# Performance work log

Measured on AMD Instinct MI355X. Metric: run time of the kernel, lower is better.

Reference implementation:

```python
import jax, jax.numpy as jnp
import numpy as np

D_MODEL = 2048
N_HEADS = 16
HEAD_DIM = D_MODEL // N_HEADS
SEGMENT_SIZE = 512
DILATION = 2
BATCH = 2
SEQ_LEN = 8192


def setup_inputs() -> dict:
    key = jax.random.key(0)
    k1, k2, k3 = jax.random.split(key, 3)
    x = jax.random.normal(k1, (BATCH, SEQ_LEN, D_MODEL), dtype=jnp.float32)
    Wqkv = jax.random.normal(k2, (3 * D_MODEL, D_MODEL), dtype=jnp.float32) * 0.02
    b_qkv = jnp.zeros((3 * D_MODEL,), dtype=jnp.float32)
    Wout = jax.random.normal(k3, (D_MODEL, D_MODEL), dtype=jnp.float32) * 0.02
    b_out = jnp.zeros((D_MODEL,), dtype=jnp.float32)
    return {"x": x, "Wqkv": Wqkv, "b_qkv": b_qkv, "Wout": Wout, "b_out": b_out}


def reference(x, Wqkv, b_qkv, Wout, b_out):
    B, S, D = x.shape
    H, hd = N_HEADS, HEAD_DIM
    # dilated segment gather: [B, n_seg, seg, D] strided by dilation -> [B, n_seg, L, D]
    xs = x.reshape(B, -1, SEGMENT_SIZE, D)[:, :, ::DILATION, :]
    N, L = xs.shape[1], xs.shape[2]
    # fused qkv projection (FlashMHA.Wqkv)
    qkv = jnp.einsum('bnld,ed->bnle', xs, Wqkv) + b_qkv  # [B,N,L,3D]
    q, k, v = jnp.split(qkv, 3, axis=-1)
    q = q.reshape(B, N, L, H, hd)
    k = k.reshape(B, N, L, H, hd)
    v = v.reshape(B, N, L, H, hd)
    scale = 1.0 / jnp.sqrt(jnp.asarray(hd, dtype=x.dtype))
    # per-segment attention over the dilated tokens
    scores = jnp.einsum('bnqhd,bnkhd->bnhqk', q, k) * scale  # [B,N,H,L,L]
    attn = jax.nn.softmax(scores, axis=-1)
    out = jnp.einsum('bnhqk,bnkhd->bnqhd', attn, v).reshape(B, N, L, D)
    # output projection (FlashMHA.out_proj)
    out = jnp.einsum('bnld,ed->bnle', out, Wout) + b_out
    # merge segments back: [B, N*L, D]
    return out.reshape(B, -1, D)
```

## Files before the change

### kernel.cpp

```cpp
#include <hip/hip_runtime.h>
#include <hip/hip_bf16.h>
#include <stdint.h>

#define DEVI __device__ __forceinline__

typedef __attribute__((ext_vector_type(8))) short bf16x8;
typedef __attribute__((ext_vector_type(4))) float f32x4;


DEVI unsigned short f2bf(float f) {
  unsigned int u = __float_as_uint(f);
  return (unsigned short)((u + 0x7fffu + ((u >> 16) & 1u)) >> 16);
}

DEVI void load_lds16(const void* g, void* l) {
  __builtin_amdgcn_global_load_lds(
      (const __attribute__((address_space(1))) unsigned int*)g,
      (__attribute__((address_space(3))) unsigned int*)l, 16, 0, 0);
}

DEVI bf16x8 ld8(const unsigned short* p) {
  return *reinterpret_cast<const bf16x8*>(p);
}

__global__ void k_gather(const float* __restrict__ x, unsigned short* __restrict__ xs) {
  int i = blockIdx.x * 256 + threadIdx.x;
  int r = i >> 9;
  int c = (i & 511) << 2;
  int b = r >> 12;
  int rem = r & 4095;
  int seg = rem >> 8;
  int lcl = rem & 255;
  long src_row = (long)b * 8192 + seg * 512 + lcl * 2;
  const float4 v = *reinterpret_cast<const float4*>(x + src_row * 2048 + c);
  uint2 o;
  o.x = f2bf(v.x) | ((unsigned)f2bf(v.y) << 16);
  o.y = f2bf(v.z) | ((unsigned)f2bf(v.w) << 16);
  *reinterpret_cast<uint2*>(xs + (long)r * 2048 + c) = o;
}

__global__ void k_cast(const float* __restrict__ in, unsigned short* __restrict__ out, int n4) {
  int i = blockIdx.x * 256 + threadIdx.x;
  if (i >= n4) return;
  const float4 v = *reinterpret_cast<const float4*>(in + (long)i * 4);
  uint2 o;
  o.x = f2bf(v.x) | ((unsigned)f2bf(v.y) << 16);
  o.y = f2bf(v.z) | ((unsigned)f2bf(v.w) << 16);
  *reinterpret_cast<uint2*>(out + (long)i * 4) = o;
}


DEVI void stage_piece(const unsigned short* gb, int K, int h, int op,
                      unsigned short* smem, int t, int w) {
  char* base = (char*)(smem + (h & 3) * 16384 + op * 8192);
#pragma unroll
  for (int i = 0; i < 2; ++i) {
    int s = i * 512 + t;
    int prow = s >> 3;
    int cs8 = s & 7;
    int c8 = cs8 ^ (prow & 7);
    int r = prow * 2 + (c8 >> 2);
    int k0 = (c8 & 3) << 3;
    load_lds16(gb + (long)r * K + h * 32 + k0, base + i * 8192 + w * 1024);
  }
}

#define FRAG_A(dst, mm)                                                      \
  { int r_ = wm * 128 + (mm) * 16 + lr;                                      \
    int p_ = r_ >> 1;                                                        \
    int cs_ = (((r_ & 1) << 2) | lq) ^ (p_ & 7);                             \
    dst = ld8(Ab_ + p_ * 64 + cs_ * 8); }
#define FRAG_B(dst, nn)                                                      \
  { int r_ = wn * 64 + (nn) * 16 + lr;                                       \
    int p_ = r_ >> 1;                                                        \
    int cs_ = (((r_ & 1) << 2) | lq) ^ (p_ & 7);                             \
    dst = ld8(Bb_ + p_ * 64 + cs_ * 8); }
#define MM(mm, areg)                                                         \
  acc[mm][0] = __builtin_amdgcn_mfma_f32_16x16x32_bf16(areg, bf0, acc[mm][0], 0, 0, 0); \
  acc[mm][1] = __builtin_amdgcn_mfma_f32_16x16x32_bf16(areg, bf1, acc[mm][1], 0, 0, 0); \
  acc[mm][2] = __builtin_amdgcn_mfma_f32_16x16x32_bf16(areg, bf2, acc[mm][2], 0, 0, 0); \
  acc[mm][3] = __builtin_amdgcn_mfma_f32_16x16x32_bf16(areg, bf3, acc[mm][3], 0, 0, 0);

#define HALF(HEXPR, DOSTAGE, VMLIT)                                          \
  {                                                                          \
    const int h_ = (HEXPR);                                                  \
    const unsigned short* Ab_ = smem + (h_ & 3) * 16384;                     \
    const unsigned short* Bb_ = Ab_ + 8192;                                  \
    bf16x8 af0, af1, af2, af3, bf0, bf1, bf2, bf3;                           \
    FRAG_B(bf0, 0) FRAG_B(bf1, 1) FRAG_B(bf2, 2) FRAG_B(bf3, 3)              \
    FRAG_A(af0, 0) FRAG_A(af1, 1) FRAG_A(af2, 2) FRAG_A(af3, 3)              \
    if (DOSTAGE) stage_piece(Agb, K, h_ + 2, 0, smem, t, w);                 \
    __builtin_amdgcn_s_barrier();                                            \
    asm volatile("s_waitcnt lgkmcnt(0)" ::: "memory");                       \
    __builtin_amdgcn_sched_barrier(0);                                       \
    __builtin_amdgcn_s_setprio(1);                                           \
    MM(0, af0) MM(1, af1) MM(2, af2) MM(3, af3)                              \
    __builtin_amdgcn_s_setprio(0);                                           \
    __builtin_amdgcn_s_barrier();                                            \
    FRAG_A(af0, 4) FRAG_A(af1, 5) FRAG_A(af2, 6) FRAG_A(af3, 7)              \
    if (DOSTAGE) stage_piece(Bgb, K, h_ + 2, 1, smem, t, w);                 \
    __builtin_amdgcn_s_barrier();                                            \
    asm volatile("s_waitcnt lgkmcnt(0)" ::: "memory");                       \
    __builtin_amdgcn_sched_barrier(0);                                       \
    __builtin_amdgcn_s_setprio(1);                                           \
    MM(4, af0) MM(5, af1) MM(6, af2) MM(7, af3)                              \
    __builtin_amdgcn_s_setprio(0);                                           \
    asm volatile("s_waitcnt vmcnt(" VMLIT ")" ::: "memory");                 \
    __builtin_amdgcn_s_barrier();                                            \
  }

template <bool BF16_OUT>
__global__ __launch_bounds__(512, 1)
void k_gemm(const unsigned short* __restrict__ A, const unsigned short* __restrict__ B,
            const float* __restrict__ bias, void* __restrict__ Cv, int N, int K) {
  __shared__ unsigned short smem[65536];
  const int nbx = N >> 8;
  const int cpx = gridDim.x >> 3;
  const int id = blockIdx.x;
  const int sw = (id & 7) * cpx + (id >> 3);
  const int bx = sw % nbx, by = sw / nbx;
  const int t = threadIdx.x, w = t >> 6, l = t & 63;
  const int lr = l & 15, lq = l >> 4;
  const int wm = w >> 2, wn = w & 3;
  const unsigned short* Agb = A + (long)by * 256 * K;
  const unsigned short* Bgb = B + (long)bx * 256 * K;
  const int nh = K >> 5;
  f32x4 acc[8][4] = {};

  stage_piece(Agb, K, 0, 0, smem, t, w);
  stage_piece(Bgb, K, 0, 1, smem, t, w);
  stage_piece(Agb, K, 1, 0, smem, t, w);
  stage_piece(Bgb, K, 1, 1, smem, t, w);
  asm volatile("s_waitcnt vmcnt(4)" ::: "memory");
  __builtin_amdgcn_s_barrier();

  for (int h = 0; h < nh - 2; ++h) HALF(h, true, "4")
  HALF(nh - 2, false, "0")
  HALF(nh - 1, false, "0")

  const long crow0 = (long)by * 256 + wm * 128;
  const int ccol0 = bx * 256 + wn * 64;
  float bv[4];
#pragma unroll
  for (int n = 0; n < 4; ++n) bv[n] = bias[ccol0 + n * 16 + lr];
  const int lrr = l >> 2;
  if (BF16_OUT) {
    unsigned short* Lw = smem + w * 1216;
    const int lcb = (l & 3) * 8;
#pragma unroll
    for (int m = 0; m < 8; ++m) {
#pragma unroll
      for (int n = 0; n < 4; ++n)
#pragma unroll
        for (int r = 0; r < 4; ++r)
          Lw[(lq * 4 + r) * 76 + n * 16 + lr] = f2bf(acc[m][n][r] + bv[n]);
      asm volatile("s_waitcnt lgkmcnt(0)" ::: "memory");
#pragma unroll
      for (int rd = 0; rd < 2; ++rd) {
        bf16x8 v = ld8(Lw + lrr * 76 + lcb + rd * 32);
        *reinterpret_cast<bf16x8*>((unsigned short*)Cv +
            (crow0 + m * 16 + lrr) * N + ccol0 + lcb + rd * 32) = v;
      }
    }
  } else {
    float* Lf = (float*)smem + w * 1216;
    const int lcf = (l & 3) * 4;
#pragma unroll
    for (int m = 0; m < 8; ++m) {
#pragma unroll
      for (int n = 0; n < 4; ++n)
#pragma unroll
        for (int r = 0; r < 4; ++r)
          Lf[(lq * 4 + r) * 76 + n * 16 + lr] = acc[m][n][r] + bv[n];
      asm volatile("s_waitcnt lgkmcnt(0)" ::: "memory");
#pragma unroll
      for (int rd = 0; rd < 4; ++rd) {
        float4 v = *reinterpret_cast<const float4*>(Lf + lrr * 76 + lcf + rd * 16);
        *reinterpret_cast<float4*>((float*)Cv +
            (crow0 + m * 16 + lrr) * N + ccol0 + lcf + rd * 16) = v;
      }
    }
  }
}

__global__ __launch_bounds__(512)
void k_attn(const unsigned short* __restrict__ qkv, unsigned short* __restrict__ aout) {
  __shared__ unsigned short smem[65536];
  unsigned short* Kl = smem;
  unsigned short* Vt = smem + 32768;
  const int p = blockIdx.x;
  const int h = p & 15;
  const long rb = (long)(p >> 4) * 256;
  const int t = threadIdx.x, w = t >> 6, l = t & 63;
  const int lr = l & 15, lq = l >> 4;

  const unsigned short* kb = qkv + rb * 6144 + 2048 + h * 128;
#pragma unroll
  for (int i = 0; i < 8; ++i) {
    int s = i * 512 + t;
    int row = s >> 4;
    int ch = (s & 15) ^ (row & 7);
    load_lds16(kb + (long)row * 6144 + ch * 8, (char*)Kl + i * 8192 + w * 1024);
  }
  const unsigned short* vb = qkv + rb * 6144 + 4096 + h * 128;
#pragma unroll
  for (int j0 = 0; j0 < 8; ++j0) {
    int k = j0 * 32 + (t >> 4);
    int d0 = (t & 15) * 8;
    bf16x8 v = ld8(vb + (long)k * 6144 + d0);
#pragma unroll
    for (int j = 0; j < 8; ++j) {
      int d = d0 + j;
      int ch = (k >> 3) ^ ((d ^ (d >> 3)) & 7);
      Vt[d * 256 + ch * 8 + (k & 7)] = (unsigned short)(short)v[j];
    }
  }
  const unsigned short* qb = qkv + (rb + w * 32) * 6144 + h * 128;
  bf16x8 qa[2][4];
#pragma unroll
  for (int m = 0; m < 2; ++m)
#pragma unroll
    for (int kt = 0; kt < 4; ++kt)
      qa[m][kt] = ld8(qb + (long)(m * 16 + lr) * 6144 + kt * 32 + lq * 8);

  __syncthreads();

  f32x4 sacc[2][16] = {};
#pragma unroll
  for (int n = 0; n < 16; ++n) {
    int row = n * 16 + lr;
#pragma unroll
    for (int kt = 0; kt < 4; ++kt) {
      int ch = (kt * 4 + lq) ^ (row & 7);
      bf16x8 kf = ld8(Kl + row * 128 + ch * 8);
      sacc[0][n] = __builtin_amdgcn_mfma_f32_16x16x32_bf16(qa[0][kt], kf, sacc[0][n], 0, 0, 0);
      sacc[1][n] = __builtin_amdgcn_mfma_f32_16x16x32_bf16(qa[1][kt], kf, sacc[1][n], 0, 0, 0);
    }
  }
  const float scale = 0.08838834764831845f;
  float mx[2][4], sm[2][4];
#pragma unroll
  for (int m = 0; m < 2; ++m)
#pragma unroll
    for (int r = 0; r < 4; ++r) {
      float v = sacc[m][0][r];
#pragma unroll
      for (int n = 1; n < 16; ++n) v = fmaxf(v, sacc[m][n][r]);
      mx[m][r] = v;
      sm[m][r] = 0.f;
    }
#pragma unroll
  for (int mk = 1; mk < 16; mk <<= 1)
#pragma unroll
    for (int m = 0; m < 2; ++m)
#pragma unroll
      for (int r = 0; r < 4; ++r)
        mx[m][r] = fmaxf(mx[m][r], __shfl_xor(mx[m][r], mk));
#pragma unroll
  for (int m = 0; m < 2; ++m)
#pragma unroll
    for (int n = 0; n < 16; ++n)
#pragma unroll
      for (int r = 0; r < 4; ++r) {
        float e = __expf((sacc[m][n][r] - mx[m][r]) * scale);
        sacc[m][n][r] = e;
        sm[m][r] += e;
      }
#pragma unroll
  for (int mk = 1; mk < 16; mk <<= 1)
#pragma unroll
    for (int m = 0; m < 2; ++m)
#pragma unroll
      for (int r = 0; r < 4; ++r)
        sm[m][r] += __shfl_xor(sm[m][r], mk);
  float ri[2][4];
#pragma unroll
  for (int m = 0; m < 2; ++m)
#pragma unroll
    for (int r = 0; r < 4; ++r) ri[m][r] = 1.0f / sm[m][r];

  unsigned int pb[2][16][2];
#pragma unroll
  for (int m = 0; m < 2; ++m)
#pragma unroll
    for (int n = 0; n < 16; ++n) {
      pb[m][n][0] = f2bf(sacc[m][n][0] * ri[m][0]) | ((unsigned)f2bf(sacc[m][n][1] * ri[m][1]) << 16);
      pb[m][n][1] = f2bf(sacc[m][n][2] * ri[m][2]) | ((unsigned)f2bf(sacc[m][n][3] * ri[m][3]) << 16);
    }

  __syncthreads();
  unsigned short* Pl = Kl + w * 4096;
  f32x4 oacc[2][8] = {};
#pragma unroll
  for (int half = 0; half < 2; ++half) {
#pragma unroll
    for (int m = 0; m < 2; ++m)
#pragma unroll
      for (int n = 0; n < 8; ++n) {
        int col = n * 16 + lr;
        int row0 = m * 16 + lq * 4;
#pragma unroll
        for (int pr = 0; pr < 2; ++pr) {
          unsigned int u = pb[m][half * 8 + n][pr];
          int ra = row0 + pr * 2, rbw = ra + 1;
          int ca = (col >> 3) ^ (ra & 7);
          int cb = (col >> 3) ^ (rbw & 7);
          Pl[ra * 128 + ca * 8 + (col & 7)] = (unsigned short)(u & 0xffffu);
          Pl[rbw * 128 + cb * 8 + (col & 7)] = (unsigned short)(u >> 16);
        }
      }
#pragma unroll
    for (int kt = 0; kt < 4; ++kt) {
      bf16x8 pa[2];
#pragma unroll
      for (int m = 0; m < 2; ++m) {
        int row = m * 16 + lr;
        int ch = (kt * 4 + lq) ^ (row & 7);
        pa[m] = ld8(Pl + row * 128 + ch * 8);
      }
#pragma unroll
      for (int dt = 0; dt < 8; ++dt) {
        int d = dt * 16 + lr;
        int kg = half * 128 + kt * 32 + lq * 8;
        int ch = (kg >> 3) ^ ((d ^ (d >> 3)) & 7);
        bf16x8 vf = ld8(Vt + d * 256 + ch * 8);
        oacc[0][dt] = __builtin_amdgcn_mfma_f32_16x16x32_bf16(pa[0], vf, oacc[0][dt], 0, 0, 0);
        oacc[1][dt] = __builtin_amdgcn_mfma_f32_16x16x32_bf16(pa[1], vf, oacc[1][dt], 0, 0, 0);
      }
    }
  }
  unsigned short* ob = aout + (rb + w * 32) * 2048 + h * 128;
#pragma unroll
  for (int m = 0; m < 2; ++m)
#pragma unroll
    for (int dt = 0; dt < 8; ++dt)
#pragma unroll
      for (int r = 0; r < 4; ++r)
        ob[(long)(m * 16 + lq * 4 + r) * 2048 + dt * 16 + lr] = f2bf(oacc[m][dt][r]);
}

extern "C" void kernel_launch(void* const* d_in, const int* in_sizes, int n_in,
                              void* d_out, int out_size, void* d_ws, size_t ws_size,
                              hipStream_t stream) {
  const float* x     = (const float*)d_in[0];
  const float* Wqkv  = (const float*)d_in[1];
  const float* b_qkv = (const float*)d_in[2];
  const float* Wout  = (const float*)d_in[3];
  const float* b_out = (const float*)d_in[4];
  float* out = (float*)d_out;

  char* ws = (char*)d_ws;
  unsigned short* xs   = (unsigned short*)(ws);
  unsigned short* aout = xs;
  unsigned short* wq   = (unsigned short*)(ws + 33554432);
  unsigned short* wo   = (unsigned short*)(ws + 58720256);
  unsigned short* qkv  = (unsigned short*)(ws + 67108864);

  k_gather<<<16384, 256, 0, stream>>>(x, xs);
  k_cast<<<12288, 256, 0, stream>>>(Wqkv, wq, 3145728);
  k_cast<<<4096, 256, 0, stream>>>(Wout, wo, 1048576);
  k_gemm<true><<<32 * 24, 512, 0, stream>>>(xs, wq, b_qkv, (void*)qkv, 6144, 2048);
  k_attn<<<512, 512, 0, stream>>>(qkv, aout);
  k_gemm<false><<<32 * 8, 512, 0, stream>>>(aout, wo, b_out, (void*)out, 2048, 2048);
}
```

Baseline: 354.3 us.

## Fuse prep kernels, deepen GEMM prefetch, and use XCD-aware tile mapping

Merges the input gather and the two weight casts into one launch to cut launch overhead. The GEMM K-loop now prefetches three stages ahead instead of two, using all four LDS slots, with waitcnt thresholds adjusted. Block-to-tile mapping now assigns each XCD a contiguous chunk of output tiles to improve L2 reuse. The deeper prefetch keeps more loads in flight, at the cost of tighter buffer reuse.

Result: faster. 341.1 us (-3.7%).

```diff
diff --git a/kernel.cpp b/kernel.cpp
--- a/kernel.cpp
+++ b/kernel.cpp
@@ -23,30 +23,40 @@
   return *reinterpret_cast<const bf16x8*>(p);
 }
 
-__global__ void k_gather(const float* __restrict__ x, unsigned short* __restrict__ xs) {
-  int i = blockIdx.x * 256 + threadIdx.x;
-  int r = i >> 9;
-  int c = (i & 511) << 2;
-  int b = r >> 12;
-  int rem = r & 4095;
-  int seg = rem >> 8;
-  int lcl = rem & 255;
-  long src_row = (long)b * 8192 + seg * 512 + lcl * 2;
-  const float4 v = *reinterpret_cast<const float4*>(x + src_row * 2048 + c);
+__global__ void k_prep(const float* __restrict__ x, unsigned short* __restrict__ xs,
+                       const float* __restrict__ Wqkv, unsigned short* __restrict__ wq,
+                       const float* __restrict__ Wout, unsigned short* __restrict__ wo) {
+  const int bid = blockIdx.x;
+  const float* src;
+  unsigned short* dst;
+  long i;
+  if (bid < 16384) {
+    int ii = bid * 256 + threadIdx.x;
+    int r = ii >> 9;
+    int c = (ii & 511) << 2;
+    int b = r >> 12;
+    int rem = r & 4095;
+    int seg = rem >> 8;
+    int lcl = rem & 255;
+    long src_row = (long)b * 8192 + seg * 512 + lcl * 2;
+    const float4 v = *reinterpret_cast<const float4*>(x + src_row * 2048 + c);
+    uint2 o;
+    o.x = f2bf(v.x) | ((unsigned)f2bf(v.y) << 16);
+    o.y = f2bf(v.z) | ((unsigned)f2bf(v.w) << 16);
+    *reinterpret_cast<uint2*>(xs + (long)r * 2048 + c) = o;
+    return;
+  } else if (bid < 28672) {
+    i = (long)(bid - 16384) * 256 + threadIdx.x;
+    src = Wqkv; dst = wq;
+  } else {
+    i = (long)(bid - 28672) * 256 + threadIdx.x;
+    src = Wout; dst = wo;
+  }
+  const float4 v = *reinterpret_cast<const float4*>(src + i * 4);
   uint2 o;
   o.x = f2bf(v.x) | ((unsigned)f2bf(v.y) << 16);
   o.y = f2bf(v.z) | ((unsigned)f2bf(v.w) << 16);
-  *reinterpret_cast<uint2*>(xs + (long)r * 2048 + c) = o;
-}
-
-__global__ void k_cast(const float* __restrict__ in, unsigned short* __restrict__ out, int n4) {
-  int i = blockIdx.x * 256 + threadIdx.x;
-  if (i >= n4) return;
-  const float4 v = *reinterpret_cast<const float4*>(in + (long)i * 4);
-  uint2 o;
-  o.x = f2bf(v.x) | ((unsigned)f2bf(v.y) << 16);
-  o.y = f2bf(v.z) | ((unsigned)f2bf(v.w) << 16);
-  *reinterpret_cast<uint2*>(out + (long)i * 4) = o;
+  *reinterpret_cast<uint2*>(dst + i * 4) = o;
 }
 
 
@@ -89,7 +99,7 @@
     bf16x8 af0, af1, af2, af3, bf0, bf1, bf2, bf3;                           \
     FRAG_B(bf0, 0) FRAG_B(bf1, 1) FRAG_B(bf2, 2) FRAG_B(bf3, 3)              \
     FRAG_A(af0, 0) FRAG_A(af1, 1) FRAG_A(af2, 2) FRAG_A(af3, 3)              \
-    if (DOSTAGE) stage_piece(Agb, K, h_ + 2, 0, smem, t, w);                 \
+    if (DOSTAGE) stage_piece(Agb, K, h_ + 3, 0, smem, t, w);                 \
     __builtin_amdgcn_s_barrier();                                            \
     asm volatile("s_waitcnt lgkmcnt(0)" ::: "memory");                       \
     __builtin_amdgcn_sched_barrier(0);                                       \
@@ -98,7 +108,7 @@
     __builtin_amdgcn_s_setprio(0);                                           \
     __builtin_amdgcn_s_barrier();                                            \
     FRAG_A(af0, 4) FRAG_A(af1, 5) FRAG_A(af2, 6) FRAG_A(af3, 7)              \
-    if (DOSTAGE) stage_piece(Bgb, K, h_ + 2, 1, smem, t, w);                 \
+    if (DOSTAGE) stage_piece(Bgb, K, h_ + 3, 1, smem, t, w);                 \
     __builtin_amdgcn_s_barrier();                                            \
     asm volatile("s_waitcnt lgkmcnt(0)" ::: "memory");                       \
     __builtin_amdgcn_sched_barrier(0);                                       \
@@ -112,13 +122,15 @@
 template <bool BF16_OUT>
 __global__ __launch_bounds__(512, 1)
 void k_gemm(const unsigned short* __restrict__ A, const unsigned short* __restrict__ B,
-            const float* __restrict__ bias, void* __restrict__ Cv, int N, int K) {
+            const float* __restrict__ bias, void* __restrict__ Cv, int N, int K,
+            int CHY, int CHX) {
   __shared__ unsigned short smem[65536];
   const int nbx = N >> 8;
-  const int cpx = gridDim.x >> 3;
-  const int id = blockIdx.x;
-  const int sw = (id & 7) * cpx + (id >> 3);
-  const int bx = sw % nbx, by = sw / nbx;
+  const int xcd = blockIdx.x & 7;
+  const int local = blockIdx.x >> 3;
+  const int nchx = nbx / CHX;
+  const int by = (xcd / nchx) * CHY + local / CHX;
+  const int bx = (xcd % nchx) * CHX + local % CHX;
   const int t = threadIdx.x, w = t >> 6, l = t & 63;
   const int lr = l & 15, lq = l >> 4;
   const int wm = w >> 2, wn = w & 3;
@@ -131,10 +143,13 @@
   stage_piece(Bgb, K, 0, 1, smem, t, w);
   stage_piece(Agb, K, 1, 0, smem, t, w);
   stage_piece(Bgb, K, 1, 1, smem, t, w);
-  asm volatile("s_waitcnt vmcnt(4)" ::: "memory");
+  stage_piece(Agb, K, 2, 0, smem, t, w);
+  stage_piece(Bgb, K, 2, 1, smem, t, w);
+  asm volatile("s_waitcnt vmcnt(8)" ::: "memory");
   __builtin_amdgcn_s_barrier();
 
-  for (int h = 0; h < nh - 2; ++h) HALF(h, true, "4")
+  for (int h = 0; h < nh - 3; ++h) HALF(h, true, "8")
+  HALF(nh - 3, false, "4")
   HALF(nh - 2, false, "0")
   HALF(nh - 1, false, "0")
 
@@ -356,10 +371,8 @@
   unsigned short* wo   = (unsigned short*)(ws + 58720256);
   unsigned short* qkv  = (unsigned short*)(ws + 67108864);
 
-  k_gather<<<16384, 256, 0, stream>>>(x, xs);
-  k_cast<<<12288, 256, 0, stream>>>(Wqkv, wq, 3145728);
-  k_cast<<<4096, 256, 0, stream>>>(Wout, wo, 1048576);
-  k_gemm<true><<<32 * 24, 512, 0, stream>>>(xs, wq, b_qkv, (void*)qkv, 6144, 2048);
+  k_prep<<<32768, 256, 0, stream>>>(x, xs, Wqkv, wq, Wout, wo);
+  k_gemm<true><<<768, 512, 0, stream>>>(xs, wq, b_qkv, (void*)qkv, 6144, 2048, 16, 6);
   k_attn<<<512, 512, 0, stream>>>(qkv, aout);
-  k_gemm<false><<<32 * 8, 512, 0, stream>>>(aout, wo, b_out, (void*)out, 2048, 2048);
-}
+  k_gemm<false><<<256, 512, 0, stream>>>(aout, wo, b_out, (void*)out, 2048, 2048, 8, 4);
+}
```
